# Optimization experiments

Measured on AMD Instinct MI355X. Metric: run time of the kernel, lower is better.

Reference implementation:

```python
import jax, jax.numpy as jnp
import numpy as np

D, H, M, FF = 1024, 16, 64, 4096
B, N, C = 8, 1024, 256


def setup_inputs() -> dict:
    key = jax.random.key(0)
    it = iter(jax.random.split(key, 24))
    def nrm(shape, s):
        return jax.random.normal(next(it), shape, dtype=jnp.float32) * s
    z = lambda *s: jnp.zeros(s, jnp.float32)
    inp = {
        'point_tokens': nrm((B, N, D), 1.0),
        'context_tokens': nrm((B, C, D), 1.0),
        'inducing': nrm((1, M, D), 0.02),
    }
    for p in ('ti', 'tp'):  # to_induced / to_points MHA
        for w in ('Wq', 'Wk', 'Wv', 'Wo'):
            inp[f'{p}_{w}'] = nrm((D, D), 0.02)
        for b in ('bq', 'bk', 'bv', 'bo'):
            inp[f'{p}_{b}'] = z(D)
    for p in ('iff', 'pff'):  # induced_ff / point_ff: LN + Linear + GELU + Linear
        inp[f'{p}_g'] = jnp.ones(D, jnp.float32); inp[f'{p}_b'] = z(D)
        inp[f'{p}_W1'] = nrm((D, FF), 0.02); inp[f'{p}_b1'] = z(FF)
        inp[f'{p}_W2'] = nrm((FF, D), 0.02); inp[f'{p}_b2'] = z(D)
    inp['ni_g'] = jnp.ones(D, jnp.float32); inp['ni_b'] = z(D)
    inp['np_g'] = jnp.ones(D, jnp.float32); inp['np_b'] = z(D)
    return inp


def layernorm(x, g, b, eps=1e-5):
    mu = x.mean(-1, keepdims=True)
    var = ((x - mu) ** 2).mean(-1, keepdims=True)
    return (x - mu) * jax.lax.rsqrt(var + eps) * g + b


def ffn(x, g, b0, W1, b1, W2, b2):
    h = layernorm(x, g, b0)
    h = jax.nn.gelu(h @ W1 + b1, approximate=False)  # torch nn.GELU default = exact erf
    return h @ W2 + b2


def mha(q, kv, Wq, bq, Wk, bk, Wv, bv, Wo, bo):
    # torch nn.MultiheadAttention semantics (batch_first, dropout=0, need_weights=True)
    Bq, Lq, Dm = q.shape
    Lk = kv.shape[1]
    hd = Dm // H
    Q = (q @ Wq + bq).reshape(Bq, Lq, H, hd)
    K = (kv @ Wk + bk).reshape(Bq, Lk, H, hd)
    V = (kv @ Wv + bv).reshape(Bq, Lk, H, hd)
    scores = jnp.einsum('bqhd,bkhd->bhqk', Q, K) / jnp.sqrt(jnp.float32(hd))
    probs = jax.nn.softmax(scores, axis=-1)
    out = jnp.einsum('bhqk,bkhd->bqhd', probs, V).reshape(Bq, Lq, Dm)
    return out @ Wo + bo, probs.mean(axis=1)  # head-averaged weights (need_weights default)


def reference(point_tokens, context_tokens, inducing,
              ti_Wq, ti_bq, ti_Wk, ti_bk, ti_Wv, ti_bv, ti_Wo, ti_bo,
              tp_Wq, tp_bq, tp_Wk, tp_bk, tp_Wv, tp_bv, tp_Wo, tp_bo,
              iff_g, iff_b, iff_W1, iff_b1, iff_W2, iff_b2,
              pff_g, pff_b, pff_W1, pff_b1, pff_W2, pff_b2,
              ni_g, ni_b, np_g, np_b):
    b = point_tokens.shape[0]
    induced = jnp.broadcast_to(inducing, (b, inducing.shape[1], inducing.shape[2]))
    kv = jnp.concatenate([context_tokens, point_tokens], axis=1)
    ia, _ = mha(induced, kv, ti_Wq, ti_bq, ti_Wk, ti_bk, ti_Wv, ti_bv, ti_Wo, ti_bo)
    induced = layernorm(induced + ia, ni_g, ni_b)
    induced = induced + ffn(induced, iff_g, iff_b, iff_W1, iff_b1, iff_W2, iff_b2)
    kv2 = jnp.concatenate([context_tokens, induced], axis=1)
    pa, w2 = mha(point_tokens, kv2, tp_Wq, tp_bq, tp_Wk, tp_bk, tp_Wv, tp_bv, tp_Wo, tp_bo)
    pts = layernorm(point_tokens + pa, np_g, np_b)
    pts = pts + ffn(pts, pff_g, pff_b, pff_W1, pff_b1, pff_W2, pff_b2)
    probs = jnp.clip(w2, 1e-8, None)
    entropy = (-(probs * jnp.log(probs)).sum(axis=-1)).mean()  # detached side output
    return pts, entropy
```

## Files before the change

### kernel.cpp

```cpp
#include <hip/hip_runtime.h>
#include <hip/hip_bf16.h>
#include <math.h>

typedef unsigned short ushort_t;
typedef __attribute__((ext_vector_type(8))) short short8;
typedef __attribute__((ext_vector_type(4))) float f32x4;

static __device__ __forceinline__ ushort_t f2b(float f){
  union{float f;unsigned u;}a; a.f=f;
  unsigned r = a.u + 0x7fffu + ((a.u>>16)&1u);
  return (ushort_t)(r>>16);
}
static __device__ __forceinline__ float b2f(ushort_t u){
  union{unsigned u;float f;}a; a.u=((unsigned)u)<<16; return a.f;
}

#define GLDS16(g,l) __builtin_amdgcn_global_load_lds((const __attribute__((address_space(1))) void*)(const void*)(g), (__attribute__((address_space(3))) void*)(void*)(l), 16, 0, 0)

template<bool GELU, int RES>
__global__ __launch_bounds__(256)
void gemm_bt(const ushort_t* __restrict__ A, const ushort_t* __restrict__ Bt,
             const float* __restrict__ bias, const void* __restrict__ Res,
             float* __restrict__ Cf, ushort_t* __restrict__ Cb,
             int M, int N, int K, int lda, int ldb, int ldres, int ldcf, int ldcb,
             int nb0,
             long sA0, long sA1, long sB0, long sB1, long sR0, long sR1,
             long sCf0, long sCf1, long sCb0, long sCb1, float scale, int resMask)
{
  const int z = blockIdx.z;
  const int b0 = z % nb0, b1 = z / nb0;
  A  += b0*sA0 + b1*sA1;
  Bt += b0*sB0 + b1*sB1;
  const float* RpF = 0; const ushort_t* RpB = 0;
  if (RES==1) RpF = (const float*)Res + b0*sR0 + b1*sR1;
  if (RES==2) RpB = (const ushort_t*)Res + b0*sR0 + b1*sR1;
  if (Cf) Cf += b0*sCf0 + b1*sCf1;
  if (Cb) Cb += b0*sCb0 + b1*sCb1;

  const int gx = gridDim.x;
  const int nwg = gx * gridDim.y;
  const int orig = blockIdx.y*gx + blockIdx.x;
  const int q8 = nwg >> 3, r8 = nwg & 7;
  const int xcd = orig & 7, ii = orig >> 3;
  const int wg = (xcd < r8 ? xcd*(q8+1) : r8*(q8+1) + (xcd-r8)*q8) + ii;
  const int bm = (wg / gx)*128, bn = (wg % gx)*128;

  __shared__ __align__(16) ushort_t As[2][4096];
  __shared__ __align__(16) ushort_t Bs[2][4096];
  const int tid = threadIdx.x, lane = tid&63, wave = tid>>6;
  const int wr = wave>>1, wc = wave&1;

  f32x4 acc[4][4] = {};

  const int c0 = wave*64 + lane;
  const int c1 = c0 + 256;
  const long rA0 = min(bm + (c0>>2), M-1);
  const long rA1 = min(bm + (c1>>2), M-1);
  const long rB0 = min(bn + (c0>>2), N-1);
  const long rB1 = min(bn + (c1>>2), N-1);
  const ushort_t* pA0 = A + rA0*lda + (c0&3)*8;
  const ushort_t* pA1 = A + rA1*lda + (c1&3)*8;
  const ushort_t* pB0 = Bt + rB0*ldb + (c0&3)*8;
  const ushort_t* pB1 = Bt + rB1*ldb + (c1&3)*8;
  const int ldsOff = wave*512;

  const int lr = lane&15, lk = (lane>>4)*8;

#define STAGE(buf, kt) do { \
    GLDS16(pA0 + (kt), &As[buf][ldsOff]); \
    GLDS16(pA1 + (kt), &As[buf][2048 + ldsOff]); \
    GLDS16(pB0 + (kt), &Bs[buf][ldsOff]); \
    GLDS16(pB1 + (kt), &Bs[buf][2048 + ldsOff]); \
  } while(0)

  STAGE(0, 0);
  __syncthreads();
  int cur = 0;
  for (int kt = 0; kt < K; kt += 32) {
    if (kt + 32 < K) STAGE(cur^1, kt+32);
    short8 af[4], bfv[4];
#pragma unroll
    for (int m=0;m<4;m++) af[m]  = *(const short8*)(&As[cur][(wr*64+m*16+lr)*32 + lk]);
#pragma unroll
    for (int n=0;n<4;n++) bfv[n] = *(const short8*)(&Bs[cur][(wc*64+n*16+lr)*32 + lk]);
#pragma unroll
    for (int m=0;m<4;m++)
#pragma unroll
      for (int n=0;n<4;n++)
        acc[m][n] = __builtin_amdgcn_mfma_f32_16x16x32_bf16(af[m], bfv[n], acc[m][n], 0, 0, 0);
    __syncthreads();
    cur ^= 1;
  }
#undef STAGE

  const int orow = bm + wr*64, ocol = bn + wc*64;
  const int rsub = (lane>>4)*4;
#pragma unroll
  for (int n=0;n<4;n++){
    const int col = ocol + n*16 + lr;
    if (col >= N) continue;
    const float bv = bias ? bias[col] : 0.f;
#pragma unroll
    for (int m=0;m<4;m++){
#pragma unroll
      for (int i=0;i<4;i++){
        const int row = orow + m*16 + rsub + i;
        if (row >= M) continue;
        float v = acc[m][n][i]*scale + bv;
        if (GELU) v = 0.5f*v*(1.f + erff(v*0.70710678118654752f));
        if (RES==1) v += RpF[(long)(row & resMask)*ldres + col];
        if (RES==2) v += b2f(RpB[(long)(row & resMask)*ldres + col]);
        if (Cf) Cf[(long)row*ldcf + col] = v;
        if (Cb) Cb[(long)row*ldcb + col] = f2b(v);
      }
    }
  }
}

template<bool WRITEP>
__global__ __launch_bounds__(256)
void fattn_k(const ushort_t* __restrict__ Qb, const ushort_t* __restrict__ KVb,
             const ushort_t* __restrict__ Vtb, ushort_t* __restrict__ Ob,
             ushort_t* __restrict__ Pb,
             int LK, int ldkv, int qRowsPerB, int oRowsPerB, float scale)
{
  const int z = blockIdx.z, b = z >> 4, h = z & 15;
  const int qt = blockIdx.x;
  const int tid = threadIdx.x, lane = tid & 63, wave = tid >> 6;
  const int lr = lane & 15, g = lane >> 4;

  __shared__ __align__(16) ushort_t Kls[64*68];
  __shared__ __align__(16) ushort_t Vtls[64*68];
  __shared__ __align__(16) ushort_t Pls[64*68];

  const long qrow = (long)b*qRowsPerB + qt*64 + wave*16 + lr;
  const short8 aq0 = *(const short8*)(Qb + qrow*1024 + h*64 + g*8);
  const short8 aq1 = *(const short8*)(Qb + qrow*1024 + h*64 + 32 + g*8);

  const ushort_t* Kbase = KVb + (long)b*LK*ldkv + h*64;
  const ushort_t* Vtbase = Vtb + (long)(b*16+h)*64*LK;

  const int ntiles = LK >> 6;
  const int r0 = tid>>3, d0c = (tid&7)*8;
  const int r1 = r0 + 32;

  float m[4] = {-3e30f,-3e30f,-3e30f,-3e30f};
  float l[4] = {0.f,0.f,0.f,0.f};

  for (int t=0; t<ntiles; ++t){
    __syncthreads();
    { short8 v0 = *(const short8*)(Kbase + (long)(t*64 + r0)*ldkv + d0c);
      short8 v1 = *(const short8*)(Kbase + (long)(t*64 + r1)*ldkv + d0c);
      *(short8*)(Kls + r0*68 + d0c) = v0;
      *(short8*)(Kls + r1*68 + d0c) = v1; }
    __syncthreads();
    f32x4 s[4];
#pragma unroll
    for(int n=0;n<4;n++){
      s[n] = (f32x4){0.f,0.f,0.f,0.f};
      short8 bk0 = *(const short8*)(Kls + (n*16+lr)*68 + g*8);
      short8 bk1 = *(const short8*)(Kls + (n*16+lr)*68 + 32 + g*8);
      s[n] = __builtin_amdgcn_mfma_f32_16x16x32_bf16(aq0, bk0, s[n],0,0,0);
      s[n] = __builtin_amdgcn_mfma_f32_16x16x32_bf16(aq1, bk1, s[n],0,0,0);
    }
#pragma unroll
    for(int i=0;i<4;i++){
      float mx = fmaxf(fmaxf(s[0][i],s[1][i]), fmaxf(s[2][i],s[3][i])) * scale;
#pragma unroll
      for(int o2=1;o2<16;o2<<=1) mx = fmaxf(mx, __shfl_xor(mx,o2));
      float mnew = fmaxf(m[i], mx);
      float sum = __expf(s[0][i]*scale-mnew)+__expf(s[1][i]*scale-mnew)
                + __expf(s[2][i]*scale-mnew)+__expf(s[3][i]*scale-mnew);
#pragma unroll
      for(int o2=1;o2<16;o2<<=1) sum += __shfl_xor(sum,o2);
      l[i] = l[i]*__expf(m[i]-mnew) + sum;
      m[i] = mnew;
    }
  }
  float invl[4];
#pragma unroll
  for(int i=0;i<4;i++) invl[i] = 1.f/l[i];

  f32x4 o[4];
#pragma unroll
  for(int n=0;n<4;n++) o[n] = (f32x4){0.f,0.f,0.f,0.f};

  long pbase = 0;
  if (WRITEP) pbase = ((long)(b*16+h)*1024 + qt*64 + wave*16)*320 + lr;

  for (int t=0; t<ntiles; ++t){
    __syncthreads();
    { short8 v0 = *(const short8*)(Kbase + (long)(t*64 + r0)*ldkv + d0c);
      short8 v1 = *(const short8*)(Kbase + (long)(t*64 + r1)*ldkv + d0c);
      short8 w0 = *(const short8*)(Vtbase + (long)r0*LK + t*64 + d0c);
      short8 w1 = *(const short8*)(Vtbase + (long)r1*LK + t*64 + d0c);
      *(short8*)(Kls + r0*68 + d0c) = v0;
      *(short8*)(Kls + r1*68 + d0c) = v1;
      *(short8*)(Vtls + r0*68 + d0c) = w0;
      *(short8*)(Vtls + r1*68 + d0c) = w1; }
    __syncthreads();
    f32x4 s[4];
#pragma unroll
    for(int n=0;n<4;n++){
      s[n] = (f32x4){0.f,0.f,0.f,0.f};
      short8 bk0 = *(const short8*)(Kls + (n*16+lr)*68 + g*8);
      short8 bk1 = *(const short8*)(Kls + (n*16+lr)*68 + 32 + g*8);
      s[n] = __builtin_amdgcn_mfma_f32_16x16x32_bf16(aq0, bk0, s[n],0,0,0);
      s[n] = __builtin_amdgcn_mfma_f32_16x16x32_bf16(aq1, bk1, s[n],0,0,0);
    }
#pragma unroll
    for(int n=0;n<4;n++){
#pragma unroll
      for(int i=0;i<4;i++){
        float e = __expf(s[n][i]*scale - m[i]);
        Pls[(wave*16 + g*4 + i)*68 + n*16 + lr] = f2b(e);
        if (WRITEP) Pb[pbase + (long)(g*4+i)*320 + t*64 + n*16] = f2b(e*invl[i]);
      }
    }
    short8 pa0 = *(const short8*)(Pls + (wave*16+lr)*68 + g*8);
    short8 pa1 = *(const short8*)(Pls + (wave*16+lr)*68 + 32 + g*8);
#pragma unroll
    for(int nd=0; nd<4; nd++){
      short8 vb0 = *(const short8*)(Vtls + (nd*16+lr)*68 + g*8);
      short8 vb1 = *(const short8*)(Vtls + (nd*16+lr)*68 + 32 + g*8);
      o[nd] = __builtin_amdgcn_mfma_f32_16x16x32_bf16(pa0, vb0, o[nd],0,0,0);
      o[nd] = __builtin_amdgcn_mfma_f32_16x16x32_bf16(pa1, vb1, o[nd],0,0,0);
    }
  }
  const long orow0 = (long)b*oRowsPerB + qt*64 + wave*16 + g*4;
#pragma unroll
  for(int nd=0;nd<4;nd++)
#pragma unroll
    for(int i=0;i<4;i++)
      Ob[(orow0+i)*1024 + h*64 + nd*16 + lr] = f2b(o[nd][i]*invl[i]);
}

__global__ __launch_bounds__(256)
void tcvt_k(const float* __restrict__ src, ushort_t* __restrict__ dst, int R, int C)
{
  __shared__ float t[32][33];
  int c0 = blockIdx.x*32, r0 = blockIdx.y*32;
  int tx = threadIdx.x & 31, ty = threadIdx.x >> 5;
  for (int i=ty;i<32;i+=8){ int r=r0+i, c=c0+tx; t[i][tx] = (r<R && c<C) ? src[(long)r*C + c] : 0.f; }
  __syncthreads();
  for (int i=ty;i<32;i+=8){ int c=c0+i, r=r0+tx; if (c<C && r<R) dst[(long)c*R + r] = f2b(t[tx][i]); }
}

__global__ __launch_bounds__(256)
void cvt_rows_k(const float* __restrict__ src, ushort_t* __restrict__ dst,
                long total, int R, long dstBS, long dstRO)
{
  long e = ((long)blockIdx.x*256 + threadIdx.x)*4;
  if (e >= total) return;
  long rc = e >> 10; int c = (int)(e & 1023);
  int r = (int)(rc % R); long b = rc / R;
  float4 v = *(const float4*)(src + e);
  ushort4 o; o.x=f2b(v.x); o.y=f2b(v.y); o.z=f2b(v.z); o.w=f2b(v.w);
  *(ushort4*)(dst + (b*dstBS + dstRO + r)*1024 + c) = o;
}

__global__ __launch_bounds__(256)
void vtrans_k(const ushort_t* __restrict__ V, ushort_t* __restrict__ Vt,
              int Lk, int ldv, int coloff)
{
  int b = blockIdx.z, h = blockIdx.y, k0 = blockIdx.x*32;
  __shared__ ushort_t t[32][65];
  int tx = threadIdx.x & 63, ty = threadIdx.x >> 6;
  for (int i=ty;i<32;i+=4) t[i][tx] = V[((long)b*Lk + k0 + i)*ldv + coloff + h*64 + tx];
  __syncthreads();
  int kk = threadIdx.x & 31, n0 = threadIdx.x >> 5;
  for (int n=n0;n<64;n+=8) Vt[((long)(b*16+h)*64 + n)*Lk + k0 + kk] = t[kk][n];
}

__global__ __launch_bounds__(256)
void ln2x_k(const float* __restrict__ x,
            const float* __restrict__ g1, const float* __restrict__ b1,
            const float* __restrict__ g2, const float* __restrict__ b2,
            float* __restrict__ y1f, ushort_t* __restrict__ y1b, ushort_t* __restrict__ y2b)
{
  const long row = blockIdx.x;
  int tid = threadIdx.x, lane = tid&63, wave = tid>>6;
  __shared__ float red[8], red2[8];
  float4 v = ((const float4*)(x + row*1024))[tid];
  float s = v.x+v.y+v.z+v.w;
  for (int o=32;o;o>>=1) s += __shfl_down(s,o);
  if (lane==0) red[wave]=s;
  __syncthreads();
  float mean = (red[0]+red[1]+red[2]+red[3])*(1.f/1024.f);
  float d0=v.x-mean, d1=v.y-mean, d2=v.z-mean, d3=v.w-mean;
  float q = d0*d0+d1*d1+d2*d2+d3*d3;
  for (int o=32;o;o>>=1) q += __shfl_down(q,o);
  if (lane==0) red[4+wave]=q;
  __syncthreads();
  float var = (red[4]+red[5]+red[6]+red[7])*(1.f/1024.f);
  float rs = rsqrtf(var+1e-5f);
  float4 gg=((const float4*)g1)[tid], bb=((const float4*)b1)[tid];
  float y0=d0*rs*gg.x+bb.x, y1v=d1*rs*gg.y+bb.y, y2v=d2*rs*gg.z+bb.z, y3=d3*rs*gg.w+bb.w;
  if (y1f) ((float4*)(y1f+row*1024))[tid] = make_float4(y0,y1v,y2v,y3);
  if (y1b){ ushort4 o4; o4.x=f2b(y0); o4.y=f2b(y1v); o4.z=f2b(y2v); o4.w=f2b(y3);
            ((ushort4*)(y1b+row*1024))[tid]=o4; }
  float s2 = y0+y1v+y2v+y3;
  for (int o=32;o;o>>=1) s2 += __shfl_down(s2,o);
  if (lane==0) red2[wave]=s2;
  __syncthreads();
  float mean2 = (red2[0]+red2[1]+red2[2]+red2[3])*(1.f/1024.f);
  float e0=y0-mean2,e1=y1v-mean2,e2=y2v-mean2,e3=y3-mean2;
  float q2 = e0*e0+e1*e1+e2*e2+e3*e3;
  for (int o=32;o;o>>=1) q2 += __shfl_down(q2,o);
  if (lane==0) red2[4+wave]=q2;
  __syncthreads();
  float var2 = (red2[4]+red2[5]+red2[6]+red2[7])*(1.f/1024.f);
  float rs2 = rsqrtf(var2+1e-5f);
  float4 g2v=((const float4*)g2)[tid], b2v=((const float4*)b2)[tid];
  ushort4 o4;
  o4.x=f2b(e0*rs2*g2v.x+b2v.x); o4.y=f2b(e1*rs2*g2v.y+b2v.y);
  o4.z=f2b(e2*rs2*g2v.z+b2v.z); o4.w=f2b(e3*rs2*g2v.w+b2v.w);
  ((ushort4*)(y2b+row*1024))[tid]=o4;
}

__global__ __launch_bounds__(256)
void w2ent_k(const ushort_t* __restrict__ P, float* __restrict__ rowent)
{
  int wid = (int)((blockIdx.x*256 + threadIdx.x) >> 6);
  int lane = threadIdx.x & 63;
  int b = wid >> 10, q = wid & 1023;
  const ushort_t* base = P + ((long)(b*16)*1024 + q)*320;
  float acc = 0.f;
#pragma unroll
  for (int j=0;j<5;j++){
    int k = j*64 + lane;
    float s = 0.f;
#pragma unroll
    for (int h=0;h<16;h++) s += b2f(base[(long)h*327680 + k]);
    float p = fmaxf(s*(1.f/16.f), 1e-8f);
    acc += p*__logf(p);
  }
  for (int o=32;o;o>>=1) acc += __shfl_down(acc, o);
  if (lane==0) rowent[wid] = acc;
}

__global__ __launch_bounds__(256)
void entfin_k(const float* __restrict__ rowent, float* __restrict__ out)
{
  float s = 0.f;
  for (int i=threadIdx.x;i<8192;i+=256) s += rowent[i];
  __shared__ float red[4];
  for (int o=32;o;o>>=1) s += __shfl_down(s,o);
  if ((threadIdx.x&63)==0) red[threadIdx.x>>6]=s;
  __syncthreads();
  if (threadIdx.x==0) out[0] = -(red[0]+red[1]+red[2]+red[3]) * (1.f/8192.f);
}

__global__ void dbg_k(float* out, float a){ out[0] = -12345.f; out[1] = a; }

static void gemm(hipStream_t s, int mode,
                 const void* A, const void* Bt, const float* bias, const void* Res,
                 void* Cf, void* Cb,
                 int M, int N, int K, int lda, int ldb, int ldres, int ldcf, int ldcb,
                 int nz, int nb0,
                 long sA0, long sA1, long sB0, long sB1, long sR0, long sR1,
                 long sCf0, long sCf1, long sCb0, long sCb1, float scale, int resMask)
{
  dim3 g((N+127)/128, (M+127)/128, nz), b(256,1,1);
#define ARGS (const ushort_t*)A,(const ushort_t*)Bt,bias,Res,(float*)Cf,(ushort_t*)Cb,M,N,K,lda,ldb,ldres,ldcf,ldcb,nb0,sA0,sA1,sB0,sB1,sR0,sR1,sCf0,sCf1,sCb0,sCb1,scale,resMask
  if      (mode == 1) gemm_bt<true ,0><<<g,b,0,s>>>(ARGS);
  else if (mode == 2) gemm_bt<false,1><<<g,b,0,s>>>(ARGS);
  else if (mode == 3) gemm_bt<false,2><<<g,b,0,s>>>(ARGS);
  else                gemm_bt<false,0><<<g,b,0,s>>>(ARGS);
#undef ARGS
}

extern "C" void kernel_launch(void* const* d_in, const int* in_sizes, int n_in,
                              void* d_out, int out_size, void* d_ws, size_t ws_size,
                              hipStream_t stream)
{
  const float* ptsIn = (const float*)d_in[0];
  const float* ctx   = (const float*)d_in[1];
  const float* induc = (const float*)d_in[2];
  const float* tiW[4]={(const float*)d_in[3],(const float*)d_in[4],(const float*)d_in[5],(const float*)d_in[6]};
  const float* tib[4]={(const float*)d_in[7],(const float*)d_in[8],(const float*)d_in[9],(const float*)d_in[10]};
  const float* tpW[4]={(const float*)d_in[11],(const float*)d_in[12],(const float*)d_in[13],(const float*)d_in[14]};
  const float* tpb[4]={(const float*)d_in[15],(const float*)d_in[16],(const float*)d_in[17],(const float*)d_in[18]};
  const float* iff_g=(const float*)d_in[19]; const float* iff_b=(const float*)d_in[20];
  const float* iffW1=(const float*)d_in[21]; const float* iff_b1=(const float*)d_in[22];
  const float* iffW2=(const float*)d_in[23]; const float* iff_b2=(const float*)d_in[24];
  const float* pff_g=(const float*)d_in[25]; const float* pff_b=(const float*)d_in[26];
  const float* pffW1=(const float*)d_in[27]; const float* pff_b1=(const float*)d_in[28];
  const float* pffW2=(const float*)d_in[29]; const float* pff_b2=(const float*)d_in[30];
  const float* ni_g=(const float*)d_in[31]; const float* ni_b=(const float*)d_in[32];
  const float* np_g=(const float*)d_in[33]; const float* np_b=(const float*)d_in[34];
  float* outF = (float*)d_out;

  char* ws = (char*)d_ws;
  size_t off = 0;
  auto alloc = [&](size_t bytes){ off=(off+255)&~(size_t)255; size_t o=off; off+=bytes; return o; };
  auto sub = [&](size_t& pp, size_t bytes){ pp=(pp+255)&~(size_t)255; size_t o=pp; pp+=bytes; return o; };

  size_t o_tiQw  = alloc(1024L*1024*2);
  size_t o_tiKVw = alloc(2048L*1024*2);
  size_t o_tiOw  = alloc(1024L*1024*2);
  size_t o_tpQw  = alloc(1024L*1024*2);
  size_t o_tpKVw = alloc(2048L*1024*2);
  size_t o_tpOw  = alloc(1024L*1024*2);
  size_t o_iffW1t = alloc(4096L*1024*2);
  size_t o_iffW2t = alloc(4096L*1024*2);
  size_t o_pffW1t = alloc(4096L*1024*2);
  size_t o_pffW2t = alloc(4096L*1024*2);
  size_t o_bti  = alloc(2048*4);
  size_t o_btp  = alloc(2048*4);
  size_t o_indb = alloc(64L*1024*2);
  size_t o_kv   = alloc(10240L*1024*2);
  size_t o_kv2  = alloc(2560L*1024*2);
  size_t o_rowent = alloc(8192*4);
  off=(off+255)&~(size_t)255;
  size_t arena = off;

  size_t p = arena;
  size_t o_Qti     = sub(p, 64L*1024*2);
  size_t o_KVti    = sub(p, 10240L*2048*2);
  size_t o_Vtti    = sub(p, 8192L*1280*2);
  size_t o_attnOti = sub(p, 512L*1024*2);
  size_t o_t1      = sub(p, 512L*1024*4);
  size_t o_ind1    = sub(p, 512L*1024*4);
  size_t o_h0i     = sub(p, 512L*1024*2);
  size_t o_h1i     = sub(p, 512L*4096*2);
  size_t need1 = p;
  p = arena;
  size_t o_attnOtp = sub(p, 8192L*1024*2);
  size_t shared = p;
  size_t o_Qtp  = sub(p, 8192L*1024*2);
  size_t o_KVtp = sub(p, 2560L*2048*2);
  size_t o_Vttp = sub(p, 8192L*320*2);
  size_t o_P    = sub(p, 8L*16*1024*320*2);
  size_t need3 = p;
  p = shared;
  size_t o_t2   = sub(p, 8192L*1024*4);
  size_t o_pts1 = sub(p, 8192L*1024*2);
  size_t o_h0p  = sub(p, 8192L*1024*2);
  size_t o_h1p  = sub(p, 8192L*4096*2);
  size_t need4 = p;

  size_t need = need1;
  if (need3>need) need=need3;
  if (need4>need) need=need4;
  if (need > ws_size){ dbg_k<<<1,1,0,stream>>>(outF, (float)(need>>20)); return; }

#define WP(o) ((void*)(ws + (o)))
#define BP(o) ((ushort_t*)(ws + (o)))
#define FP(o) ((float*)(ws + (o)))
  const long Z0[10] = {0,0,0,0,0,0,0,0,0,0};

  tcvt_k<<<dim3(32,32),256,0,stream>>>(tiW[0], BP(o_tiQw), 1024, 1024);
  tcvt_k<<<dim3(32,32),256,0,stream>>>(tiW[1], BP(o_tiKVw), 1024, 1024);
  tcvt_k<<<dim3(32,32),256,0,stream>>>(tiW[2], BP(o_tiKVw) + 1024L*1024, 1024, 1024);
  tcvt_k<<<dim3(32,32),256,0,stream>>>(tiW[3], BP(o_tiOw), 1024, 1024);
  tcvt_k<<<dim3(32,32),256,0,stream>>>(tpW[0], BP(o_tpQw), 1024, 1024);
  tcvt_k<<<dim3(32,32),256,0,stream>>>(tpW[1], BP(o_tpKVw), 1024, 1024);
  tcvt_k<<<dim3(32,32),256,0,stream>>>(tpW[2], BP(o_tpKVw) + 1024L*1024, 1024, 1024);
  tcvt_k<<<dim3(32,32),256,0,stream>>>(tpW[3], BP(o_tpOw), 1024, 1024);
  tcvt_k<<<dim3(128,32),256,0,stream>>>(iffW1, BP(o_iffW1t), 1024, 4096);
  tcvt_k<<<dim3(32,128),256,0,stream>>>(iffW2, BP(o_iffW2t), 4096, 1024);
  tcvt_k<<<dim3(128,32),256,0,stream>>>(pffW1, BP(o_pffW1t), 1024, 4096);
  tcvt_k<<<dim3(32,128),256,0,stream>>>(pffW2, BP(o_pffW2t), 4096, 1024);
  hipMemcpyAsync(WP(o_bti), (const void*)tib[1], 1024*4, hipMemcpyDeviceToDevice, stream);
  hipMemcpyAsync((void*)(ws+o_bti+1024*4), (const void*)tib[2], 1024*4, hipMemcpyDeviceToDevice, stream);
  hipMemcpyAsync(WP(o_btp), (const void*)tpb[1], 1024*4, hipMemcpyDeviceToDevice, stream);
  hipMemcpyAsync((void*)(ws+o_btp+1024*4), (const void*)tpb[2], 1024*4, hipMemcpyDeviceToDevice, stream);

  cvt_rows_k<<<2048,256,0,stream>>>(ctx,   BP(o_kv),  8L*256*1024, 256, 1280, 0);
  cvt_rows_k<<<8192,256,0,stream>>>(ptsIn, BP(o_kv),  8L*1024*1024, 1024, 1280, 256);
  cvt_rows_k<<<64,256,0,stream>>>(induc,   BP(o_indb), 64L*1024, 64, 64, 0);
  cvt_rows_k<<<2048,256,0,stream>>>(ctx,   BP(o_kv2), 8L*256*1024, 256, 320, 0);

  gemm(stream,0, WP(o_indb), WP(o_tiQw), tib[0], 0, 0, WP(o_Qti),
       64,1024,1024, 1024,1024,0,0,1024, 1,1, 0,0,0,0,0,0,0,0,0,0, 1.f,-1);
  gemm(stream,0, WP(o_kv), WP(o_tiKVw), FP(o_bti), 0, 0, WP(o_KVti),
       10240,2048,1024, 1024,1024,0,0,2048, 1,1, 0,0,0,0,0,0,0,0,0,0, 1.f,-1);
  vtrans_k<<<dim3(40,16,8),256,0,stream>>>(BP(o_KVti), BP(o_Vtti), 1280, 2048, 1024);
  fattn_k<false><<<dim3(1,1,128),256,0,stream>>>(BP(o_Qti), BP(o_KVti), BP(o_Vtti),
       BP(o_attnOti), (ushort_t*)0, 1280, 2048, 0, 64, 0.125f);
  gemm(stream,2, WP(o_attnOti), WP(o_tiOw), tib[3], (const void*)induc, WP(o_t1), 0,
       512,1024,1024, 1024,1024,1024,1024,0, 1,1, 0,0,0,0,0,0,0,0,0,0, 1.f,63);
  ln2x_k<<<512,256,0,stream>>>(FP(o_t1), ni_g, ni_b, iff_g, iff_b, FP(o_ind1), 0, BP(o_h0i));
  gemm(stream,1, WP(o_h0i), WP(o_iffW1t), iff_b1, 0, 0, WP(o_h1i),
       512,4096,1024, 1024,1024,0,0,4096, 1,1, 0,0,0,0,0,0,0,0,0,0, 1.f,-1);
  gemm(stream,2, WP(o_h1i), WP(o_iffW2t), iff_b2, WP(o_ind1), 0, BP(o_kv2) + 262144,
       64,1024,4096, 4096,4096,1024,0,1024, 8,8,
       262144,0, 0,0, 65536,0, 0,0, 327680,0, 1.f,-1);

  gemm(stream,0, BP(o_kv) + 262144, WP(o_tpQw), tpb[0], 0, 0, WP(o_Qtp),
       1024,1024,1024, 1024,1024,0,0,1024, 8,8,
       1310720,0, 0,0, 0,0, 0,0, 1048576,0, 1.f,-1);
  gemm(stream,0, WP(o_kv2), WP(o_tpKVw), FP(o_btp), 0, 0, WP(o_KVtp),
       2560,2048,1024, 1024,1024,0,0,2048, 1,1, 0,0,0,0,0,0,0,0,0,0, 1.f,-1);
  vtrans_k<<<dim3(10,16,8),256,0,stream>>>(BP(o_KVtp), BP(o_Vttp), 320, 2048, 1024);
  fattn_k<true><<<dim3(16,1,128),256,0,stream>>>(BP(o_Qtp), BP(o_KVtp), BP(o_Vttp),
       BP(o_attnOtp), BP(o_P), 320, 2048, 1024, 1024, 0.125f);
  w2ent_k<<<2048,256,0,stream>>>(BP(o_P), FP(o_rowent));
  entfin_k<<<1,256,0,stream>>>(FP(o_rowent), outF + (out_size-1));
  gemm(stream,2, WP(o_attnOtp), WP(o_tpOw), tpb[3], (const void*)ptsIn, WP(o_t2), 0,
       8192,1024,1024, 1024,1024,1024,1024,0, 1,1, 0,0,0,0,0,0,0,0,0,0, 1.f,-1);
  ln2x_k<<<8192,256,0,stream>>>(FP(o_t2), np_g, np_b, pff_g, pff_b, 0, BP(o_pts1), BP(o_h0p));
  gemm(stream,1, WP(o_h0p), WP(o_pffW1t), pff_b1, 0, 0, WP(o_h1p),
       8192,4096,1024, 1024,1024,0,0,4096, 1,1, 0,0,0,0,0,0,0,0,0,0, 1.f,-1);
  gemm(stream,3, WP(o_h1p), WP(o_pffW2t), pff_b2, WP(o_pts1), outF, 0,
       8192,1024,4096, 4096,4096,1024,1024,0, 1,1, 0,0,0,0,0,0,0,0,0,0, 1.f,-1);

  (void)Z0;
#undef WP
#undef BP
#undef FP
}
```

Measured before the change: 927.9 us.

## Add 256x128-tile 512-thread GEMM with XCD remapping for large projections

Adds a new bf16 MFMA GEMM kernel that uses 256x128 output tiles with 8 waves, double-buffered LDS filled by direct global-to-LDS loads, XOR-swizzled LDS reads, and a workgroup remap that groups tiles per XCD. The large GEMMs (KV projections, point Q projection, output projection, and both point FFN layers) now use it in place of the 128x128 kernel. The aim is more data reuse per tile, overlap of loads with MFMA work, and better L2 locality across XCDs. In exchange the kernel uses 96KB of LDS, which limits occupancy, and some GEMMs now launch fewer workgroups.

```diff
diff --git a/kernel.cpp b/kernel.cpp
--- a/kernel.cpp
+++ b/kernel.cpp
@@ -16,6 +16,144 @@
 }
 
 #define GLDS16(g,l) __builtin_amdgcn_global_load_lds((const __attribute__((address_space(1))) void*)(const void*)(g), (__attribute__((address_space(3))) void*)(void*)(l), 16, 0, 0)
+
+template<bool GELU, int RES>
+__global__ __launch_bounds__(512)
+void gemm256(const ushort_t* __restrict__ A, const ushort_t* __restrict__ Bt,
+             const float* __restrict__ bias, const void* __restrict__ Res,
+             float* __restrict__ Cf, ushort_t* __restrict__ Cb,
+             int M, int N, int K, int lda, int ldb, int ldres, int ldcf, int ldcb,
+             int nb0,
+             long sA0, long sA1, long sB0, long sB1, long sR0, long sR1,
+             long sCf0, long sCf1, long sCb0, long sCb1, float scale)
+{
+  const int z = blockIdx.z;
+  const int zb0 = z % nb0, zb1 = z / nb0;
+  A  += zb0*sA0 + zb1*sA1;
+  Bt += zb0*sB0 + zb1*sB1;
+  const float* RpF = 0; const ushort_t* RpB = 0;
+  if (RES==1) RpF = (const float*)Res + zb0*sR0 + zb1*sR1;
+  if (RES==2) RpB = (const ushort_t*)Res + zb0*sR0 + zb1*sR1;
+  if (Cf) Cf += zb0*sCf0 + zb1*sCf1;
+  if (Cb) Cb += zb0*sCb0 + zb1*sCb1;
+
+  const int gx = gridDim.x;
+  const int nwg = gx * gridDim.y;
+  const int orig = blockIdx.y*gx + blockIdx.x;
+  const int q8 = nwg >> 3, r8 = nwg & 7;
+  const int xcd = orig & 7, ii = orig >> 3;
+  const int wg = (xcd < r8 ? xcd*(q8+1) : r8*(q8+1) + (xcd-r8)*q8) + ii;
+  const int bm = (wg / gx)*256, bn = (wg % gx)*128;
+
+  __shared__ __align__(16) char AsR[2][32768];
+  __shared__ __align__(16) char BsR[2][16384];
+
+  const int tid = threadIdx.x, lane = tid&63, w = tid>>6;
+  const int wr = w>>1, wc = w&1;
+  const int lr = lane&15, g16 = (lane>>4)*16;
+  const int rxor = (lr&7)<<4;
+
+  f32x4 acc[4][4] = {};
+
+  const int colElem = ((lane&7) ^ ((lane>>3)&7)) << 3;
+  const int srRow = w*8 + (lane>>3);
+  const ushort_t* pAst[4];
+  const ushort_t* pBst[2];
+#pragma unroll
+  for (int a=0;a<4;a++){
+    long r = min((long)(bm + a*64 + srRow), (long)M-1);
+    pAst[a] = A + r*lda + colElem;
+  }
+#pragma unroll
+  for (int b=0;b<2;b++){
+    long r = min((long)(bn + b*64 + srRow), (long)N-1);
+    pBst[b] = Bt + r*ldb + colElem;
+  }
+
+  const int aOff = (wr*64 + lr)*128;
+  const int bOff = (wc*64 + lr)*128;
+  const int NT = K >> 6;
+
+#pragma unroll
+  for (int a=0;a<4;a++) GLDS16(pAst[a], AsR[0] + a*8192 + w*1024);
+#pragma unroll
+  for (int b=0;b<2;b++) GLDS16(pBst[b], BsR[0] + b*8192 + w*1024);
+  asm volatile("s_waitcnt vmcnt(0)" ::: "memory");
+  __builtin_amdgcn_s_barrier();
+
+  for (int t=0; t<NT; ++t){
+    const char* Ab = AsR[t&1];
+    const char* Bb = BsR[t&1];
+    char* Abn = AsR[(t&1)^1];
+    char* Bbn = BsR[(t&1)^1];
+    const long ktn = (long)(t+1)<<6;
+    short8 a0[4], b0[4], a1[4], b1[4];
+
+#pragma unroll
+    for (int m=0;m<4;m++) a0[m] = *(const short8*)(Ab + aOff + m*2048 + (g16 ^ rxor));
+#pragma unroll
+    for (int n=0;n<4;n++) b0[n] = *(const short8*)(Bb + bOff + n*2048 + (g16 ^ rxor));
+    if (t+1 < NT){
+#pragma unroll
+      for (int a=0;a<4;a++) GLDS16(pAst[a] + ktn, Abn + a*8192 + w*1024);
+#pragma unroll
+      for (int b=0;b<2;b++) GLDS16(pBst[b] + ktn, Bbn + b*8192 + w*1024);
+    }
+    __builtin_amdgcn_s_barrier();
+    asm volatile("s_waitcnt lgkmcnt(0)" ::: "memory");
+    __builtin_amdgcn_sched_barrier(0);
+    __builtin_amdgcn_s_setprio(1);
+#pragma unroll
+    for (int m=0;m<4;m++)
+#pragma unroll
+      for (int n=0;n<4;n++)
+        acc[m][n] = __builtin_amdgcn_mfma_f32_16x16x32_bf16(a0[m], b0[n], acc[m][n],0,0,0);
+    __builtin_amdgcn_s_setprio(0);
+    __builtin_amdgcn_sched_barrier(0);
+    __builtin_amdgcn_s_barrier();
+
+#pragma unroll
+    for (int m=0;m<4;m++) a1[m] = *(const short8*)(Ab + aOff + m*2048 + ((64 + g16) ^ rxor));
+#pragma unroll
+    for (int n=0;n<4;n++) b1[n] = *(const short8*)(Bb + bOff + n*2048 + ((64 + g16) ^ rxor));
+    __builtin_amdgcn_s_barrier();
+    asm volatile("s_waitcnt lgkmcnt(0)" ::: "memory");
+    __builtin_amdgcn_sched_barrier(0);
+    __builtin_amdgcn_s_setprio(1);
+#pragma unroll
+    for (int m=0;m<4;m++)
+#pragma unroll
+      for (int n=0;n<4;n++)
+        acc[m][n] = __builtin_amdgcn_mfma_f32_16x16x32_bf16(a1[m], b1[n], acc[m][n],0,0,0);
+    __builtin_amdgcn_s_setprio(0);
+    __builtin_amdgcn_sched_barrier(0);
+    asm volatile("s_waitcnt vmcnt(0)" ::: "memory");
+    __builtin_amdgcn_s_barrier();
+  }
+
+  const int orow = bm + wr*64, ocol = bn + wc*64;
+  const int rsub = (lane>>4)*4;
+#pragma unroll
+  for (int n=0;n<4;n++){
+    const int col = ocol + n*16 + lr;
+    if (col >= N) continue;
+    const float bv = bias ? bias[col] : 0.f;
+#pragma unroll
+    for (int m=0;m<4;m++){
+#pragma unroll
+      for (int i=0;i<4;i++){
+        const int row = orow + m*16 + rsub + i;
+        if (row >= M) continue;
+        float v = acc[m][n][i]*scale + bv;
+        if (GELU) v = 0.5f*v*(1.f + erff(v*0.70710678118654752f));
+        if (RES==1) v += RpF[(long)row*ldres + col];
+        if (RES==2) v += b2f(RpB[(long)row*ldres + col]);
+        if (Cf) Cf[(long)row*ldcf + col] = v;
+        if (Cb) Cb[(long)row*ldcb + col] = f2b(v);
+      }
+    }
+  }
+}
 
 template<bool GELU, int RES>
 __global__ __launch_bounds__(256)
@@ -367,6 +505,23 @@
   else if (mode == 2) gemm_bt<false,1><<<g,b,0,s>>>(ARGS);
   else if (mode == 3) gemm_bt<false,2><<<g,b,0,s>>>(ARGS);
   else                gemm_bt<false,0><<<g,b,0,s>>>(ARGS);
+#undef ARGS
+}
+
+static void g256(hipStream_t s, int mode,
+                 const void* A, const void* Bt, const float* bias, const void* Res,
+                 void* Cf, void* Cb,
+                 int M, int N, int K, int lda, int ldb, int ldres, int ldcf, int ldcb,
+                 int nz, int nb0,
+                 long sA0, long sA1, long sB0, long sB1, long sR0, long sR1,
+                 long sCf0, long sCf1, long sCb0, long sCb1, float scale)
+{
+  dim3 g((N+127)/128, (M+255)/256, nz), b(512,1,1);
+#define ARGS (const ushort_t*)A,(const ushort_t*)Bt,bias,Res,(float*)Cf,(ushort_t*)Cb,M,N,K,lda,ldb,ldres,ldcf,ldcb,nb0,sA0,sA1,sB0,sB1,sR0,sR1,sCf0,sCf1,sCb0,sCb1,scale
+  if      (mode == 1) gemm256<true ,0><<<g,b,0,s>>>(ARGS);
+  else if (mode == 2) gemm256<false,1><<<g,b,0,s>>>(ARGS);
+  else if (mode == 3) gemm256<false,2><<<g,b,0,s>>>(ARGS);
+  else                gemm256<false,0><<<g,b,0,s>>>(ARGS);
 #undef ARGS
 }
 
@@ -448,7 +603,6 @@
 #define WP(o) ((void*)(ws + (o)))
 #define BP(o) ((ushort_t*)(ws + (o)))
 #define FP(o) ((float*)(ws + (o)))
-  const long Z0[10] = {0,0,0,0,0,0,0,0,0,0};
 
   tcvt_k<<<dim3(32,32),256,0,stream>>>(tiW[0], BP(o_tiQw), 1024, 1024);
   tcvt_k<<<dim3(32,32),256,0,stream>>>(tiW[1], BP(o_tiKVw), 1024, 1024);
@@ -474,8 +628,8 @@
 
   gemm(stream,0, WP(o_indb), WP(o_tiQw), tib[0], 0, 0, WP(o_Qti),
        64,1024,1024, 1024,1024,0,0,1024, 1,1, 0,0,0,0,0,0,0,0,0,0, 1.f,-1);
-  gemm(stream,0, WP(o_kv), WP(o_tiKVw), FP(o_bti), 0, 0, WP(o_KVti),
-       10240,2048,1024, 1024,1024,0,0,2048, 1,1, 0,0,0,0,0,0,0,0,0,0, 1.f,-1);
+  g256(stream,0, WP(o_kv), WP(o_tiKVw), FP(o_bti), 0, 0, WP(o_KVti),
+       10240,2048,1024, 1024,1024,0,0,2048, 1,1, 0,0,0,0,0,0,0,0,0,0, 1.f);
   vtrans_k<<<dim3(40,16,8),256,0,stream>>>(BP(o_KVti), BP(o_Vtti), 1280, 2048, 1024);
   fattn_k<false><<<dim3(1,1,128),256,0,stream>>>(BP(o_Qti), BP(o_KVti), BP(o_Vtti),
        BP(o_attnOti), (ushort_t*)0, 1280, 2048, 0, 64, 0.125f);
@@ -488,25 +642,24 @@
        64,1024,4096, 4096,4096,1024,0,1024, 8,8,
        262144,0, 0,0, 65536,0, 0,0, 327680,0, 1.f,-1);
 
-  gemm(stream,0, BP(o_kv) + 262144, WP(o_tpQw), tpb[0], 0, 0, WP(o_Qtp),
+  g256(stream,0, BP(o_kv) + 262144, WP(o_tpQw), tpb[0], 0, 0, WP(o_Qtp),
        1024,1024,1024, 1024,1024,0,0,1024, 8,8,
-       1310720,0, 0,0, 0,0, 0,0, 1048576,0, 1.f,-1);
-  gemm(stream,0, WP(o_kv2), WP(o_tpKVw), FP(o_btp), 0, 0, WP(o_KVtp),
-       2560,2048,1024, 1024,1024,0,0,2048, 1,1, 0,0,0,0,0,0,0,0,0,0, 1.f,-1);
+       1310720,0, 0,0, 0,0, 0,0, 1048576,0, 1.f);
+  g256(stream,0, WP(o_kv2), WP(o_tpKVw), FP(o_btp), 0, 0, WP(o_KVtp),
+       2560,2048,1024, 1024,1024,0,0,2048, 1,1, 0,0,0,0,0,0,0,0,0,0, 1.f);
   vtrans_k<<<dim3(10,16,8),256,0,stream>>>(BP(o_KVtp), BP(o_Vttp), 320, 2048, 1024);
   fattn_k<true><<<dim3(16,1,128),256,0,stream>>>(BP(o_Qtp), BP(o_KVtp), BP(o_Vttp),
        BP(o_attnOtp), BP(o_P), 320, 2048, 1024, 1024, 0.125f);
   w2ent_k<<<2048,256,0,stream>>>(BP(o_P), FP(o_rowent));
   entfin_k<<<1,256,0,stream>>>(FP(o_rowent), outF + (out_size-1));
-  gemm(stream,2, WP(o_attnOtp), WP(o_tpOw), tpb[3], (const void*)ptsIn, WP(o_t2), 0,
-       8192,1024,1024, 1024,1024,1024,1024,0, 1,1, 0,0,0,0,0,0,0,0,0,0, 1.f,-1);
+  g256(stream,2, WP(o_attnOtp), WP(o_tpOw), tpb[3], (const void*)ptsIn, WP(o_t2), 0,
+       8192,1024,1024, 1024,1024,1024,1024,0, 1,1, 0,0,0,0,0,0,0,0,0,0, 1.f);
   ln2x_k<<<8192,256,0,stream>>>(FP(o_t2), np_g, np_b, pff_g, pff_b, 0, BP(o_pts1), BP(o_h0p));
-  gemm(stream,1, WP(o_h0p), WP(o_pffW1t), pff_b1, 0, 0, WP(o_h1p),
-       8192,4096,1024, 1024,1024,0,0,4096, 1,1, 0,0,0,0,0,0,0,0,0,0, 1.f,-1);
-  gemm(stream,3, WP(o_h1p), WP(o_pffW2t), pff_b2, WP(o_pts1), outF, 0,
-       8192,1024,4096, 4096,4096,1024,1024,0, 1,1, 0,0,0,0,0,0,0,0,0,0, 1.f,-1);
-
-  (void)Z0;
+  g256(stream,1, WP(o_h0p), WP(o_pffW1t), pff_b1, 0, 0, WP(o_h1p),
+       8192,4096,1024, 1024,1024,0,0,4096, 1,1, 0,0,0,0,0,0,0,0,0,0, 1.f);
+  g256(stream,3, WP(o_h1p), WP(o_pffW2t), pff_b2, WP(o_pts1), outF, 0,
+       8192,1024,4096, 4096,4096,1024,1024,0, 1,1, 0,0,0,0,0,0,0,0,0,0, 1.f);
+
 #undef WP
 #undef BP
 #undef FP
```

Result: slower. 954.9 us (+2.9%).
